# Kernel tuning notes

Hardware: AMD Instinct MI355X
Metric: run time of the kernel (lower is better)

Reference implementation:

```python
import jax, jax.numpy as jnp
import numpy as np

B, T, C = 2, 2048, 2048
N_HEAD, N_KV = 32, 8
HD = C // N_HEAD  # 64
N_REP = N_HEAD // N_KV  # 4
ROPE_BASE = 10000.0


def setup_inputs() -> dict:
    key = jax.random.key(0)
    ks = jax.random.split(key, 5)
    s = 0.02
    return {
        "x": jax.random.normal(ks[0], (B, T, C), jnp.float32),
        "Wq": jax.random.normal(ks[1], (C, N_HEAD * HD), jnp.float32) * s,
        "Wk": jax.random.normal(ks[2], (C, N_KV * HD), jnp.float32) * s,
        "Wv": jax.random.normal(ks[3], (C, N_KV * HD), jnp.float32) * s,
        "Wo": jax.random.normal(ks[4], (N_HEAD * HD, C), jnp.float32) * s,
    }


def _rope_cos_sin(seq_len, head_dim, dtype):
    inv_freq = 1.0 / (ROPE_BASE ** (jnp.arange(0, head_dim, 2, dtype=jnp.float32) / head_dim))
    t = jnp.arange(seq_len, dtype=jnp.float32)
    freqs = t[:, None] * inv_freq[None, :]           # (T, hd/2)
    emb = jnp.concatenate([freqs, freqs], axis=-1)    # (T, hd)
    return jnp.cos(emb).astype(dtype), jnp.sin(emb).astype(dtype)


def _rotate_half(x):
    h = x.shape[-1] // 2
    return jnp.concatenate([-x[..., h:], x[..., :h]], axis=-1)


def reference(x, Wq, Wk, Wv, Wo):
    b, t, c = x.shape
    # projections -> (B, H, T, hd)
    q = (x @ Wq).reshape(b, t, N_HEAD, HD).transpose(0, 2, 1, 3)
    k = (x @ Wk).reshape(b, t, N_KV, HD).transpose(0, 2, 1, 3)
    v = (x @ Wv).reshape(b, t, N_KV, HD).transpose(0, 2, 1, 3)

    cos, sin = _rope_cos_sin(t, HD, x.dtype)          # (T, hd)
    q = q * cos + _rotate_half(q) * sin
    k = k * cos + _rotate_half(k) * sin

    # GQA: group query heads (B, n_kv, n_rep, T, hd) against shared KV (no repeat materialization)
    qg = q.reshape(b, N_KV, N_REP, t, HD)
    scale = 1.0 / jnp.sqrt(jnp.asarray(HD, x.dtype))
    scores = jnp.einsum('bgrqd,bgkd->bgrqk', qg, k) * scale  # (B, n_kv, n_rep, T, T)
    causal = jnp.tril(jnp.ones((t, t), bool))
    scores = jnp.where(causal, scores, jnp.asarray(-jnp.inf, scores.dtype))
    probs = jax.nn.softmax(scores, axis=-1)
    out = jnp.einsum('bgrqk,bgkd->bgrqd', probs, v)          # (B, n_kv, n_rep, T, hd)
    out = out.reshape(b, N_HEAD, t, HD).transpose(0, 2, 1, 3).reshape(b, t, N_HEAD * HD)
    return out @ Wo
```

## Files before the change

### kernel.cpp

```cpp
#include <hip/hip_runtime.h>
#include <stdint.h>

#define Bn 2
#define Tn 2048
#define Cn 2048
#define NHEAD 32
#define NKVH 8
#define HDIM 64
#define Mn (Bn*Tn)
#define NQKV 3072
#define KOFF 2048
#define VOFF 2560

typedef __attribute__((ext_vector_type(8))) short bf16x8;
typedef __attribute__((ext_vector_type(4))) float f32x4;

#define AS1 __attribute__((address_space(1)))
#define AS3 __attribute__((address_space(3)))
#define GLOAD_LDS16(g, l) __builtin_amdgcn_global_load_lds((const AS1 void*)(g), (AS3 void*)(l), 16, 0, 0)

#define SCL 0.18033688f

#define SYNC_FENCE() __builtin_amdgcn_sched_barrier(0)
#define WAIT_VM8()  do { asm volatile("s_waitcnt vmcnt(8)" ::: "memory"); SYNC_FENCE(); } while (0)
#define WAIT_VM0()  do { asm volatile("s_waitcnt vmcnt(0)" ::: "memory"); SYNC_FENCE(); } while (0)
#define BARRIER_RAW() do { __builtin_amdgcn_s_barrier(); SYNC_FENCE(); } while (0)

__device__ __forceinline__ unsigned short f2bf(float f) {
    union { float f; unsigned u; } v; v.f = f;
    return (unsigned short)((v.u + 0x7fffu + ((v.u >> 16) & 1u)) >> 16);
}
__device__ __forceinline__ float bf2f(unsigned short b) {
    union { unsigned u; float f; } v; v.u = ((unsigned)b) << 16;
    return v.f;
}

__global__ void convert_f32_bf16(const float* __restrict__ src,
                                 unsigned short* __restrict__ dst, int n4) {
    int i = blockIdx.x * blockDim.x + threadIdx.x;
    if (i >= n4) return;
    float4 f = ((const float4*)src)[i];
    ushort4 o;
    o.x = f2bf(f.x); o.y = f2bf(f.y); o.z = f2bf(f.z); o.w = f2bf(f.w);
    ((ushort4*)dst)[i] = o;
}

__global__ void transpose_convert(const float* __restrict__ src,
                                  unsigned short* __restrict__ dst, int K, int N) {
    __shared__ float tile[32][33];
    int k0 = blockIdx.x * 32, n0 = blockIdx.y * 32;
    int tx = threadIdx.x, ty = threadIdx.y;
    #pragma unroll
    for (int yy = 0; yy < 32; yy += 8)
        tile[ty + yy][tx] = src[(size_t)(k0 + ty + yy) * N + n0 + tx];
    __syncthreads();
    #pragma unroll
    for (int yy = 0; yy < 32; yy += 8)
        dst[(size_t)(n0 + ty + yy) * K + k0 + tx] = f2bf(tile[tx][ty + yy]);
}

__global__ void transpose_wqkv(const float* __restrict__ Wq, const float* __restrict__ Wk,
                               const float* __restrict__ Wv, unsigned short* __restrict__ dst) {
    __shared__ float tile[32][33];
    int k0 = blockIdx.x * 32, n0 = blockIdx.y * 32;
    const float* src; int srcN, c0;
    if (n0 < 2048)      { src = Wq; srcN = 2048; c0 = n0; }
    else if (n0 < 2560) { src = Wk; srcN = 512;  c0 = n0 - 2048; }
    else                { src = Wv; srcN = 512;  c0 = n0 - 2560; }
    int tx = threadIdx.x, ty = threadIdx.y;
    #pragma unroll
    for (int yy = 0; yy < 32; yy += 8)
        tile[ty + yy][tx] = src[(size_t)(k0 + ty + yy) * srcN + c0 + tx];
    __syncthreads();
    #pragma unroll
    for (int yy = 0; yy < 32; yy += 8)
        dst[(size_t)(n0 + ty + yy) * Cn + k0 + tx] = f2bf(tile[tx][ty + yy]);
}

__global__ void rope_tables(float* __restrict__ ct, float* __restrict__ st) {
    int i = blockIdx.x * blockDim.x + threadIdx.x;
    int t = i >> 5, d = i & 31;
    float invf = powf(10000.0f, -(float)d / 32.0f);
    float f = (float)t * invf;
    ct[i] = cosf(f);
    st[i] = sinf(f);
}

__global__ void transpose_v(const unsigned short* __restrict__ qkv,
                            unsigned short* __restrict__ vt) {
    __shared__ unsigned short tile[32][33];
    int t0 = blockIdx.x * 32;
    int b = blockIdx.y >> 3, kvh = blockIdx.y & 7;
    int d0 = blockIdx.z * 32;
    int tx = threadIdx.x, ty = threadIdx.y;
    #pragma unroll
    for (int yy = 0; yy < 32; yy += 8)
        tile[ty + yy][tx] = qkv[(size_t)(b * Tn + t0 + ty + yy) * NQKV + VOFF + kvh * 64 + d0 + tx];
    __syncthreads();
    #pragma unroll
    for (int yy = 0; yy < 32; yy += 8)
        vt[(size_t)((b * 8 + kvh) * 64 + d0 + ty + yy) * Tn + t0 + tx] = tile[tx][ty + yy];
}

template <int BM, int BN, int WMv, int WNv, bool ROPE>
__global__ __launch_bounds__(WMv * WNv * 64, 2) void gemm_pipe(
    const unsigned short* __restrict__ A, const unsigned short* __restrict__ Bt,
    unsigned short* __restrict__ outb, float* __restrict__ outf, int N, int K,
    const float* __restrict__ ct, const float* __restrict__ st) {
    constexpr int THREADS = WMv * WNv * 64;
    constexpr int MR = BM / WMv / 16;
    constexpr int NR = BN / WNv / 16;
    constexpr int LOADS = (BM * 64 * 2) / (THREADS * 16);

    __shared__ unsigned short sA[2][BM * 64];
    __shared__ unsigned short sB[2][BN * 64];

    int tid = threadIdx.x;
    int wid = tid >> 6, lane = tid & 63;
    int wm = wid / WNv, wn = wid % WNv;
    int g = lane >> 4, r16 = lane & 15;

    int nwg = gridDim.x * gridDim.y;
    int lid = blockIdx.y * gridDim.x + blockIdx.x;
    int swz = (lid & 7) * (nwg >> 3) + (lid >> 3);
    int bx = swz % gridDim.x, by = swz / gridDim.x;
    int brow = by * BM, bcol = bx * BN;

    int NT = K / 64;

    auto stage = [&](int kt, int b) {
        #pragma unroll
        for (int li = 0; li < LOADS; li++) {
            int cb = li * (THREADS * 16) + wid * 1024;
            int bo = cb + lane * 16;
            int row = bo >> 7;
            int coff = (bo & 127) ^ ((row & 7) << 4);
            GLOAD_LDS16(A + (size_t)(brow + row) * K + kt * 64 + (coff >> 1),
                        (char*)&sA[b][0] + cb);
            GLOAD_LDS16(Bt + (size_t)(bcol + row) * K + kt * 64 + (coff >> 1),
                        (char*)&sB[b][0] + cb);
        }
    };

    f32x4 acc[MR][NR];
    #pragma unroll
    for (int m = 0; m < MR; m++)
        #pragma unroll
        for (int n = 0; n < NR; n++) acc[m][n] = (f32x4){0.f, 0.f, 0.f, 0.f};

    stage(0, 0);
    stage(1, 1);

    for (int kt = 0; kt < NT; kt++) {
        if (kt + 1 < NT) { WAIT_VM8(); } else { WAIT_VM0(); }
        BARRIER_RAW();
        const char* cA = (const char*)&sA[kt & 1][0];
        const char* cB = (const char*)&sB[kt & 1][0];
        bf16x8 av[MR][2];
        #pragma unroll
        for (int m = 0; m < MR; m++)
            #pragma unroll
            for (int kc = 0; kc < 2; kc++) {
                int row = wm * (MR * 16) + m * 16 + r16;
                int byo = (row * 128 + kc * 64 + g * 16) ^ ((row & 7) << 4);
                av[m][kc] = *(const bf16x8*)(cA + byo);
            }
        #pragma unroll
        for (int n = 0; n < NR; n++) {
            bf16x8 bv[2];
            #pragma unroll
            for (int kc = 0; kc < 2; kc++) {
                int row = wn * (NR * 16) + n * 16 + r16;
                int byo = (row * 128 + kc * 64 + g * 16) ^ ((row & 7) << 4);
                bv[kc] = *(const bf16x8*)(cB + byo);
            }
            __builtin_amdgcn_s_setprio(1);
            #pragma unroll
            for (int m = 0; m < MR; m++)
                #pragma unroll
                for (int kc = 0; kc < 2; kc++)
                    acc[m][n] = __builtin_amdgcn_mfma_f32_16x16x32_bf16(av[m][kc], bv[kc], acc[m][n], 0, 0, 0);
            __builtin_amdgcn_s_setprio(0);
        }
        BARRIER_RAW();
        if (kt + 2 < NT) stage(kt + 2, kt & 1);
        SYNC_FENCE();
    }

    if (ROPE) {
        #pragma unroll
        for (int m = 0; m < MR; m++) {
            #pragma unroll
            for (int n = 0; n < NR / 2; n++) {
                int col = bcol + wn * (NR * 16) + n * 16 + r16;
                int p = col & 63;
                bool isV = (col >= VOFF);
                float scl = (col < KOFF) ? SCL : 1.0f;
                #pragma unroll
                for (int r = 0; r < 4; r++) {
                    int row = brow + wm * (MR * 16) + m * 16 + g * 4 + r;
                    int tt = row & (Tn - 1);
                    float v0 = acc[m][n][r], v1 = acc[m][n + NR / 2][r];
                    float o0, o1;
                    if (isV) { o0 = v0; o1 = v1; }
                    else {
                        float c = ct[tt * 32 + p], s = st[tt * 32 + p];
                        o0 = (v0 * c - v1 * s) * scl;
                        o1 = (v1 * c + v0 * s) * scl;
                    }
                    outb[(size_t)row * N + col]      = f2bf(o0);
                    outb[(size_t)row * N + col + 32] = f2bf(o1);
                }
            }
        }
    } else {
        #pragma unroll
        for (int m = 0; m < MR; m++) {
            #pragma unroll
            for (int n = 0; n < NR; n++) {
                int row0 = brow + wm * (MR * 16) + m * 16 + g * 4;
                int col = bcol + wn * (NR * 16) + n * 16 + r16;
                #pragma unroll
                for (int r = 0; r < 4; r++)
                    outf[(size_t)(row0 + r) * N + col] = acc[m][n][r];
            }
        }
    }
}

__device__ __forceinline__ void flash_step(
    const bf16x8 (&qf)[2], float (&pl)[4], f32x4 (&oo)[4],
    const unsigned short* __restrict__ sK, const unsigned short* __restrict__ sVt,
    unsigned short* __restrict__ sPw, int g, int r16, int wid, bool masked) {
    f32x4 s[4];
    __builtin_amdgcn_s_setprio(1);
    #pragma unroll
    for (int n = 0; n < 4; n++) {
        s[n] = (f32x4){0.f, 0.f, 0.f, 0.f};
        #pragma unroll
        for (int kc = 0; kc < 2; kc++) {
            int kv = n * 16 + r16;
            int bo = (kv * 128 + kc * 64 + g * 16) ^ ((kv & 7) << 4);
            bf16x8 kf = *(const bf16x8*)((const char*)sK + bo);
            s[n] = __builtin_amdgcn_mfma_f32_16x16x32_bf16(qf[kc], kf, s[n], 0, 0, 0);
        }
    }
    __builtin_amdgcn_s_setprio(0);
    if (masked) {
        #pragma unroll
        for (int n = 0; n < 4; n++)
            #pragma unroll
            for (int r = 0; r < 4; r++)
                s[n][r] = (n * 16 + r16 <= wid * 16 + g * 4 + r) ? s[n][r] : -1e30f;
    }
    #pragma unroll
    for (int n = 0; n < 4; n++)
        #pragma unroll
        for (int r = 0; r < 4; r++) s[n][r] = exp2f(s[n][r]);
    #pragma unroll
    for (int r = 0; r < 4; r++)
        pl[r] += (s[0][r] + s[1][r]) + (s[2][r] + s[3][r]);
    #pragma unroll
    for (int n = 0; n < 4; n++)
        #pragma unroll
        for (int r = 0; r < 4; r++) {
            int prow = g * 4 + r;
            int bo = (prow * 128 + (n * 16 + r16) * 2) ^ ((prow & 7) << 4);
            union { float f; unsigned u; } pv; pv.f = s[n][r];
            *(unsigned short*)((char*)sPw + bo) = (unsigned short)(pv.u >> 16);
        }
    __builtin_amdgcn_s_setprio(1);
    #pragma unroll
    for (int dt = 0; dt < 4; dt++) {
        #pragma unroll
        for (int kc = 0; kc < 2; kc++) {
            int bo = (r16 * 128 + kc * 64 + g * 16) ^ ((r16 & 7) << 4);
            bf16x8 pf = *(const bf16x8*)((const char*)sPw + bo);
            int dd = dt * 16 + r16;
            int bo2 = (dd * 128 + kc * 64 + g * 16) ^ ((dd & 7) << 4);
            bf16x8 vf = *(const bf16x8*)((const char*)sVt + bo2);
            oo[dt] = __builtin_amdgcn_mfma_f32_16x16x32_bf16(pf, vf, oo[dt], 0, 0, 0);
        }
    }
    __builtin_amdgcn_s_setprio(0);
}

__global__ __launch_bounds__(256, 4) void attn_fwd(
    const unsigned short* __restrict__ qkv, const unsigned short* __restrict__ vt,
    unsigned short* __restrict__ att) {
    __shared__ unsigned short sK[2][64 * 64];
    __shared__ unsigned short sVt[2][64 * 64];
    __shared__ unsigned short sP[4][16 * 64];

    int tid = threadIdx.x;
    int wid = tid >> 6, lane = tid & 63;
    int g = lane >> 4, r16 = lane & 15;
    int qp = blockIdx.x;
    int bh = blockIdx.y;
    int b = bh >> 5, qh = bh & 31, kvh = qh >> 2;
    int qtA = qp, qtB = 31 - qp;

    const unsigned short* base = qkv + (size_t)b * Tn * NQKV;
    const unsigned short* kg = base + KOFF + kvh * 64;
    const unsigned short* vg = vt + (size_t)((b * 8 + kvh) * 64) * Tn;

    bf16x8 qfA[2], qfB[2];
    {
        int qrA = qtA * 64 + wid * 16 + r16;
        int qrB = qtB * 64 + wid * 16 + r16;
        #pragma unroll
        for (int kc = 0; kc < 2; kc++) {
            qfA[kc] = *(const bf16x8*)(base + (size_t)qrA * NQKV + qh * 64 + kc * 32 + g * 8);
            qfB[kc] = *(const bf16x8*)(base + (size_t)qrB * NQKV + qh * 64 + kc * 32 + g * 8);
        }
    }

    float plA[4], plB[4];
    f32x4 oA[4], oB[4];
    #pragma unroll
    for (int r = 0; r < 4; r++) { plA[r] = 0.f; plB[r] = 0.f; }
    #pragma unroll
    for (int d = 0; d < 4; d++) {
        oA[d] = (f32x4){0.f, 0.f, 0.f, 0.f};
        oB[d] = (f32x4){0.f, 0.f, 0.f, 0.f};
    }

    unsigned short* sPw = &sP[wid][0];

    #pragma unroll
    for (int jj = 0; jj < 2; jj++) {
        int c = wid * 2 + jj;
        int bo = c * 1024 + lane * 16;
        int row = bo >> 7;
        int coff = (bo & 127) ^ ((row & 7) << 4);
        GLOAD_LDS16(kg + (size_t)row * NQKV + (coff >> 1), (char*)&sK[0][0] + c * 1024);
        GLOAD_LDS16(vg + (size_t)row * Tn + (coff >> 1), (char*)&sVt[0][0] + c * 1024);
    }
    __syncthreads();

    int cur = 0;
    for (int j = 0; j <= qtB; j++) {
        if (j < qtB) {
            int nxt = cur ^ 1;
            #pragma unroll
            for (int jj = 0; jj < 2; jj++) {
                int c = wid * 2 + jj;
                int bo = c * 1024 + lane * 16;
                int row = bo >> 7;
                int coff = (bo & 127) ^ ((row & 7) << 4);
                GLOAD_LDS16(kg + (size_t)((j + 1) * 64 + row) * NQKV + (coff >> 1),
                            (char*)&sK[nxt][0] + c * 1024);
                GLOAD_LDS16(vg + (size_t)row * Tn + (j + 1) * 64 + (coff >> 1),
                            (char*)&sVt[nxt][0] + c * 1024);
            }
        }
        const unsigned short* sKc = &sK[cur][0];
        const unsigned short* sVc = &sVt[cur][0];
        if (j <= qtA) flash_step(qfA, plA, oA, sKc, sVc, sPw, g, r16, wid, j == qtA);
        flash_step(qfB, plB, oB, sKc, sVc, sPw, g, r16, wid, j == qtB);
        __syncthreads();
        cur ^= 1;
    }

    float lA[4], lB[4];
    #pragma unroll
    for (int r = 0; r < 4; r++) {
        float vA = plA[r], vB = plB[r];
        #pragma unroll
        for (int msk = 1; msk < 16; msk <<= 1) {
            vA += __shfl_xor(vA, msk, 64);
            vB += __shfl_xor(vB, msk, 64);
        }
        lA[r] = 1.0f / vA;
        lB[r] = 1.0f / vB;
    }
    #pragma unroll
    for (int dt = 0; dt < 4; dt++)
        #pragma unroll
        for (int r = 0; r < 4; r++) {
            int qgA = qtA * 64 + wid * 16 + g * 4 + r;
            int qgB = qtB * 64 + wid * 16 + g * 4 + r;
            att[(size_t)(b * Tn + qgA) * Cn + qh * 64 + dt * 16 + r16] = f2bf(oA[dt][r] * lA[r]);
            att[(size_t)(b * Tn + qgB) * Cn + qh * 64 + dt * 16 + r16] = f2bf(oB[dt][r] * lB[r]);
        }
}

extern "C" void kernel_launch(void* const* d_in, const int* in_sizes, int n_in,
                              void* d_out, int out_size, void* d_ws, size_t ws_size,
                              hipStream_t stream) {
    const float* x  = (const float*)d_in[0];
    const float* Wq = (const float*)d_in[1];
    const float* Wk = (const float*)d_in[2];
    const float* Wv = (const float*)d_in[3];
    const float* Wo = (const float*)d_in[4];
    float* out = (float*)d_out;

    char* w = (char*)d_ws;
    unsigned short* Xb    = (unsigned short*)w; w += (size_t)Mn * Cn * 2;
    unsigned short* Wqkvt = (unsigned short*)w; w += (size_t)NQKV * Cn * 2;
    unsigned short* Wot   = (unsigned short*)w; w += (size_t)Cn * Cn * 2;
    unsigned short* QKV   = (unsigned short*)w; w += (size_t)Mn * NQKV * 2;
    unsigned short* ATT   = (unsigned short*)w; w += (size_t)Mn * Cn * 2;
    unsigned short* Vt    = (unsigned short*)w; w += (size_t)Bn * NKVH * HDIM * Tn * 2;
    float* ct = (float*)w; w += (size_t)Tn * 32 * 4;
    float* st = (float*)w; w += (size_t)Tn * 32 * 4;

    convert_f32_bf16<<<(Mn * Cn / 4) / 256, 256, 0, stream>>>(x, Xb, Mn * Cn / 4);
    dim3 tb(32, 8);
    transpose_wqkv<<<dim3(64, 96), tb, 0, stream>>>(Wq, Wk, Wv, Wqkvt);
    transpose_convert<<<dim3(64, 64), tb, 0, stream>>>(Wo, Wot, Cn, 2048);
    rope_tables<<<(Tn * 32) / 256, 256, 0, stream>>>(ct, st);

    gemm_pipe<256, 256, 2, 4, true><<<dim3(NQKV / 256, Mn / 256), 512, 0, stream>>>(
        Xb, Wqkvt, QKV, nullptr, NQKV, Cn, ct, st);
    transpose_v<<<dim3(Tn / 32, Bn * NKVH, 2), tb, 0, stream>>>(QKV, Vt);
    attn_fwd<<<dim3(16, Bn * NHEAD), 256, 0, stream>>>(QKV, Vt, ATT);
    gemm_pipe<128, 128, 2, 2, false><<<dim3(Cn / 128, Mn / 128), 256, 0, stream>>>(
        ATT, Wot, nullptr, out, Cn, Cn, nullptr, nullptr);
}
```

Measured before the change: 223.8 us.

## Rewrite QKV GEMM with phased quarter-tile MFMA schedule interleaving global loads

Replaces the templated 256x256 QKV projection GEMM with a dedicated kernel. It splits each K-tile into four quadrant MFMA phases and issues half-tile global-to-LDS loads for the next stage between phases, with barriers and LDS waits around each phase. The aim is finer overlap of memory traffic with MFMA work and fewer register-held fragments at once. The cost is many more barriers per tile, plus a full vmcnt(0) wait at each tile boundary that could serialize loads. The output projection GEMM is split into its own non-template copy with no functional change.

```diff
diff --git a/kernel.cpp b/kernel.cpp
--- a/kernel.cpp
+++ b/kernel.cpp
@@ -22,8 +22,9 @@
 #define SCL 0.18033688f
 
 #define SYNC_FENCE() __builtin_amdgcn_sched_barrier(0)
-#define WAIT_VM8()  do { asm volatile("s_waitcnt vmcnt(8)" ::: "memory"); SYNC_FENCE(); } while (0)
-#define WAIT_VM0()  do { asm volatile("s_waitcnt vmcnt(0)" ::: "memory"); SYNC_FENCE(); } while (0)
+#define WAIT_VM8()   do { asm volatile("s_waitcnt vmcnt(8)" ::: "memory"); SYNC_FENCE(); } while (0)
+#define WAIT_VM0()   do { asm volatile("s_waitcnt vmcnt(0)" ::: "memory"); SYNC_FENCE(); } while (0)
+#define WAIT_LGKM0() do { asm volatile("s_waitcnt lgkmcnt(0)" ::: "memory"); SYNC_FENCE(); } while (0)
 #define BARRIER_RAW() do { __builtin_amdgcn_s_barrier(); SYNC_FENCE(); } while (0)
 
 __device__ __forceinline__ unsigned short f2bf(float f) {
@@ -102,36 +103,171 @@
         vt[(size_t)((b * 8 + kvh) * 64 + d0 + ty + yy) * Tn + t0 + tx] = tile[tx][ty + yy];
 }
 
-template <int BM, int BN, int WMv, int WNv, bool ROPE>
-__global__ __launch_bounds__(WMv * WNv * 64, 2) void gemm_pipe(
+#define MFMA_Q(MH, NH, AV, BV) do { \
+    __builtin_amdgcn_s_setprio(1); \
+    _Pragma("unroll") for (int n_ = 0; n_ < 2; n_++) \
+    _Pragma("unroll") for (int m_ = 0; m_ < 4; m_++) \
+    _Pragma("unroll") for (int kc_ = 0; kc_ < 2; kc_++) \
+        acc[(MH) * 4 + m_][(NH) * 2 + n_] = __builtin_amdgcn_mfma_f32_16x16x32_bf16( \
+            AV[m_][kc_], BV[n_][kc_], acc[(MH) * 4 + m_][(NH) * 2 + n_], 0, 0, 0); \
+    __builtin_amdgcn_s_setprio(0); \
+} while (0)
+
+#define TILE4(SLOT, ST_EN, ST_KT) do { \
+    const char* cSA = (const char*)&sA[SLOT][0]; \
+    const char* cSB = (const char*)&sB[SLOT][0]; \
+     \
+    load_av(av0, cSA, 0); load_bv(bv, cSB, 0); \
+    if (ST_EN) stage_half(A, sA, (SLOT) ^ 1, brow, ST_KT, 0); \
+    BARRIER_RAW(); WAIT_LGKM0(); \
+    MFMA_Q(0, 0, av0, bv); \
+    BARRIER_RAW(); \
+     \
+    load_av(av1, cSA, 1); \
+    if (ST_EN) stage_half(A, sA, (SLOT) ^ 1, brow, ST_KT, 1); \
+    BARRIER_RAW(); WAIT_LGKM0(); \
+    MFMA_Q(1, 0, av1, bv); \
+    BARRIER_RAW(); \
+     \
+    load_bv(bv, cSB, 1); \
+    if (ST_EN) stage_half(Bt, sB, (SLOT) ^ 1, bcol, ST_KT, 0); \
+    BARRIER_RAW(); WAIT_LGKM0(); \
+    MFMA_Q(0, 1, av0, bv); \
+    BARRIER_RAW(); \
+     \
+    if (ST_EN) stage_half(Bt, sB, (SLOT) ^ 1, bcol, ST_KT, 1); \
+    BARRIER_RAW(); \
+    MFMA_Q(1, 1, av1, bv); \
+} while (0)
+
+__global__ __launch_bounds__(512, 2) void gemm256_8ph(
     const unsigned short* __restrict__ A, const unsigned short* __restrict__ Bt,
-    unsigned short* __restrict__ outb, float* __restrict__ outf, int N, int K,
+    unsigned short* __restrict__ outb,
     const float* __restrict__ ct, const float* __restrict__ st) {
-    constexpr int THREADS = WMv * WNv * 64;
-    constexpr int MR = BM / WMv / 16;
-    constexpr int NR = BN / WNv / 16;
-    constexpr int LOADS = (BM * 64 * 2) / (THREADS * 16);
-
-    __shared__ unsigned short sA[2][BM * 64];
-    __shared__ unsigned short sB[2][BN * 64];
-
+    __shared__ unsigned short sA[2][256 * 64];
+    __shared__ unsigned short sB[2][256 * 64];
     int tid = threadIdx.x;
     int wid = tid >> 6, lane = tid & 63;
-    int wm = wid / WNv, wn = wid % WNv;
+    int wm = wid >> 2, wn = wid & 3;
     int g = lane >> 4, r16 = lane & 15;
 
     int nwg = gridDim.x * gridDim.y;
     int lid = blockIdx.y * gridDim.x + blockIdx.x;
     int swz = (lid & 7) * (nwg >> 3) + (lid >> 3);
     int bx = swz % gridDim.x, by = swz / gridDim.x;
-    int brow = by * BM, bcol = bx * BN;
+    int brow = by * 256, bcol = bx * 256;
+
+    const int NT = Cn / 64;
+
+    auto stage_half = [&](const unsigned short* __restrict__ src, unsigned short (*dst)[256 * 64],
+                          int sl, int base_row, int kt, int h) {
+        #pragma unroll
+        for (int r = 0; r < 2; r++) {
+            int off = h * 16384 + r * 8192 + wid * 1024 + lane * 16;
+            int row = off >> 7;
+            int coff = (off & 127) ^ ((row & 7) << 4);
+            GLOAD_LDS16(src + (size_t)(base_row + row) * Cn + kt * 64 + (coff >> 1),
+                        (char*)&dst[sl][0] + h * 16384 + r * 8192 + wid * 1024);
+        }
+    };
+    auto load_av = [&](bf16x8 (&av)[4][2], const char* cS, int mh) {
+        #pragma unroll
+        for (int m = 0; m < 4; m++)
+            #pragma unroll
+            for (int kc = 0; kc < 2; kc++) {
+                int row = wm * 128 + mh * 64 + m * 16 + r16;
+                int byo = (row * 128 + kc * 64 + g * 16) ^ ((row & 7) << 4);
+                av[m][kc] = *(const bf16x8*)(cS + byo);
+            }
+    };
+    auto load_bv = [&](bf16x8 (&bv)[2][2], const char* cS, int nh) {
+        #pragma unroll
+        for (int n = 0; n < 2; n++)
+            #pragma unroll
+            for (int kc = 0; kc < 2; kc++) {
+                int row = wn * 64 + nh * 32 + n * 16 + r16;
+                int byo = (row * 128 + kc * 64 + g * 16) ^ ((row & 7) << 4);
+                bv[n][kc] = *(const bf16x8*)(cS + byo);
+            }
+    };
+
+    f32x4 acc[8][4];
+    #pragma unroll
+    for (int m = 0; m < 8; m++)
+        #pragma unroll
+        for (int n = 0; n < 4; n++) acc[m][n] = (f32x4){0.f, 0.f, 0.f, 0.f};
+    bf16x8 av0[4][2], av1[4][2], bv[2][2];
+
+    #pragma unroll
+    for (int h = 0; h < 2; h++) {
+        stage_half(A, sA, 0, brow, 0, h);
+        stage_half(Bt, sB, 0, bcol, 0, h);
+    }
+    WAIT_VM0();
+    BARRIER_RAW();
+
+    for (int i = 0; i < NT / 2; i++) {
+        int t0 = 2 * i;
+        TILE4(0, true, t0 + 1);
+        WAIT_VM0();
+        BARRIER_RAW();
+        bool en = (t0 + 2 < NT);
+        TILE4(1, en, t0 + 2);
+        WAIT_VM0();
+        BARRIER_RAW();
+    }
+
+    #pragma unroll
+    for (int m = 0; m < 8; m++) {
+        #pragma unroll
+        for (int n = 0; n < 2; n++) {
+            int col = bcol + wn * 64 + n * 16 + r16;
+            int p = col & 63;
+            bool isV = (col >= VOFF);
+            float scl = (col < KOFF) ? SCL : 1.0f;
+            #pragma unroll
+            for (int r = 0; r < 4; r++) {
+                int row = brow + wm * 128 + m * 16 + g * 4 + r;
+                int tt = row & (Tn - 1);
+                float v0 = acc[m][n][r], v1 = acc[m][n + 2][r];
+                float o0, o1;
+                if (isV) { o0 = v0; o1 = v1; }
+                else {
+                    float c = ct[tt * 32 + p], s = st[tt * 32 + p];
+                    o0 = (v0 * c - v1 * s) * scl;
+                    o1 = (v1 * c + v0 * s) * scl;
+                }
+                outb[(size_t)row * NQKV + col]      = f2bf(o0);
+                outb[(size_t)row * NQKV + col + 32] = f2bf(o1);
+            }
+        }
+    }
+}
+
+__global__ __launch_bounds__(256, 2) void gemm_pipe128(
+    const unsigned short* __restrict__ A, const unsigned short* __restrict__ Bt,
+    float* __restrict__ outf, int N, int K) {
+    constexpr int MR = 4, NR = 4, LOADS = 4;
+    __shared__ unsigned short sA[2][128 * 64];
+    __shared__ unsigned short sB[2][128 * 64];
+
+    int tid = threadIdx.x;
+    int wid = tid >> 6, lane = tid & 63;
+    int wm = wid >> 1, wn = wid & 1;
+    int g = lane >> 4, r16 = lane & 15;
+
+    int nwg = gridDim.x * gridDim.y;
+    int lid = blockIdx.y * gridDim.x + blockIdx.x;
+    int swz = (lid & 7) * (nwg >> 3) + (lid >> 3);
+    int bx = swz % gridDim.x, by = swz / gridDim.x;
+    int brow = by * 128, bcol = bx * 128;
 
     int NT = K / 64;
 
     auto stage = [&](int kt, int b) {
         #pragma unroll
         for (int li = 0; li < LOADS; li++) {
-            int cb = li * (THREADS * 16) + wid * 1024;
+            int cb = li * 4096 + wid * 1024;
             int bo = cb + lane * 16;
             int row = bo >> 7;
             int coff = (bo & 127) ^ ((row & 7) << 4);
@@ -161,25 +297,25 @@
         for (int m = 0; m < MR; m++)
             #pragma unroll
             for (int kc = 0; kc < 2; kc++) {
-                int row = wm * (MR * 16) + m * 16 + r16;
+                int row = wm * 64 + m * 16 + r16;
                 int byo = (row * 128 + kc * 64 + g * 16) ^ ((row & 7) << 4);
                 av[m][kc] = *(const bf16x8*)(cA + byo);
             }
         #pragma unroll
         for (int n = 0; n < NR; n++) {
-            bf16x8 bv[2];
+            bf16x8 bvv[2];
             #pragma unroll
             for (int kc = 0; kc < 2; kc++) {
-                int row = wn * (NR * 16) + n * 16 + r16;
+                int row = wn * 64 + n * 16 + r16;
                 int byo = (row * 128 + kc * 64 + g * 16) ^ ((row & 7) << 4);
-                bv[kc] = *(const bf16x8*)(cB + byo);
+                bvv[kc] = *(const bf16x8*)(cB + byo);
             }
             __builtin_amdgcn_s_setprio(1);
             #pragma unroll
             for (int m = 0; m < MR; m++)
                 #pragma unroll
                 for (int kc = 0; kc < 2; kc++)
-                    acc[m][n] = __builtin_amdgcn_mfma_f32_16x16x32_bf16(av[m][kc], bv[kc], acc[m][n], 0, 0, 0);
+                    acc[m][n] = __builtin_amdgcn_mfma_f32_16x16x32_bf16(av[m][kc], bvv[kc], acc[m][n], 0, 0, 0);
             __builtin_amdgcn_s_setprio(0);
         }
         BARRIER_RAW();
@@ -187,45 +323,16 @@
         SYNC_FENCE();
     }
 
-    if (ROPE) {
-        #pragma unroll
-        for (int m = 0; m < MR; m++) {
-            #pragma unroll
-            for (int n = 0; n < NR / 2; n++) {
-                int col = bcol + wn * (NR * 16) + n * 16 + r16;
-                int p = col & 63;
-                bool isV = (col >= VOFF);
-                float scl = (col < KOFF) ? SCL : 1.0f;
-                #pragma unroll
-                for (int r = 0; r < 4; r++) {
-                    int row = brow + wm * (MR * 16) + m * 16 + g * 4 + r;
-                    int tt = row & (Tn - 1);
-                    float v0 = acc[m][n][r], v1 = acc[m][n + NR / 2][r];
-                    float o0, o1;
-                    if (isV) { o0 = v0; o1 = v1; }
-                    else {
-                        float c = ct[tt * 32 + p], s = st[tt * 32 + p];
-                        o0 = (v0 * c - v1 * s) * scl;
-                        o1 = (v1 * c + v0 * s) * scl;
-                    }
-                    outb[(size_t)row * N + col]      = f2bf(o0);
-                    outb[(size_t)row * N + col + 32] = f2bf(o1);
-                }
-            }
-        }
-    } else {
-        #pragma unroll
-        for (int m = 0; m < MR; m++) {
-            #pragma unroll
-            for (int n = 0; n < NR; n++) {
-                int row0 = brow + wm * (MR * 16) + m * 16 + g * 4;
-                int col = bcol + wn * (NR * 16) + n * 16 + r16;
-                #pragma unroll
-                for (int r = 0; r < 4; r++)
-                    outf[(size_t)(row0 + r) * N + col] = acc[m][n][r];
-            }
-        }
-    }
+    #pragma unroll
+    for (int m = 0; m < MR; m++)
+        #pragma unroll
+        for (int n = 0; n < NR; n++) {
+            int row0 = brow + wm * 64 + m * 16 + g * 4;
+            int col = bcol + wn * 64 + n * 16 + r16;
+            #pragma unroll
+            for (int r = 0; r < 4; r++)
+                outf[(size_t)(row0 + r) * N + col] = acc[m][n][r];
+        }
 }
 
 __device__ __forceinline__ void flash_step(
@@ -411,10 +518,8 @@
     transpose_convert<<<dim3(64, 64), tb, 0, stream>>>(Wo, Wot, Cn, 2048);
     rope_tables<<<(Tn * 32) / 256, 256, 0, stream>>>(ct, st);
 
-    gemm_pipe<256, 256, 2, 4, true><<<dim3(NQKV / 256, Mn / 256), 512, 0, stream>>>(
-        Xb, Wqkvt, QKV, nullptr, NQKV, Cn, ct, st);
+    gemm256_8ph<<<dim3(NQKV / 256, Mn / 256), 512, 0, stream>>>(Xb, Wqkvt, QKV, ct, st);
     transpose_v<<<dim3(Tn / 32, Bn * NKVH, 2), tb, 0, stream>>>(QKV, Vt);
     attn_fwd<<<dim3(16, Bn * NHEAD), 256, 0, stream>>>(QKV, Vt, ATT);
-    gemm_pipe<128, 128, 2, 2, false><<<dim3(Cn / 128, Mn / 128), 256, 0, stream>>>(
-        ATT, Wot, nullptr, out, Cn, Cn, nullptr, nullptr);
-}
+    gemm_pipe128<<<dim3(Cn / 128, Mn / 128), 256, 0, stream>>>(ATT, Wot, out, Cn, Cn);
+}
```

New measurement: 241.6 us. 1.08x slower.

## Read K and V tiles directly from global memory in attention, dropping LDS staging

Applied to the files above, without the earlier changes.

The attention kernel no longer stages K and V^T tiles into double-buffered shared memory with async global-to-LDS loads and per-tile barriers. Each wave now loads its MFMA fragments for K and V straight from global memory (through cache) on every step, and the s_setprio hints are removed. This removes the block-wide barriers and the LDS footprint but makes every wave re-fetch the same K/V data and exposes global-load latency to the MFMA chain without explicit prefetch.

```diff
diff --git a/kernel.cpp b/kernel.cpp
--- a/kernel.cpp
+++ b/kernel.cpp
@@ -230,22 +230,18 @@
 
 __device__ __forceinline__ void flash_step(
     const bf16x8 (&qf)[2], float (&pl)[4], f32x4 (&oo)[4],
-    const unsigned short* __restrict__ sK, const unsigned short* __restrict__ sVt,
-    unsigned short* __restrict__ sPw, int g, int r16, int wid, bool masked) {
+    const unsigned short* __restrict__ kg, const unsigned short* __restrict__ vg,
+    unsigned short* __restrict__ sPw, int j, int g, int r16, int wid, bool masked) {
     f32x4 s[4];
-    __builtin_amdgcn_s_setprio(1);
     #pragma unroll
     for (int n = 0; n < 4; n++) {
         s[n] = (f32x4){0.f, 0.f, 0.f, 0.f};
         #pragma unroll
         for (int kc = 0; kc < 2; kc++) {
-            int kv = n * 16 + r16;
-            int bo = (kv * 128 + kc * 64 + g * 16) ^ ((kv & 7) << 4);
-            bf16x8 kf = *(const bf16x8*)((const char*)sK + bo);
+            const bf16x8 kf = *(const bf16x8*)(kg + (size_t)(j * 64 + n * 16 + r16) * NQKV + kc * 32 + g * 8);
             s[n] = __builtin_amdgcn_mfma_f32_16x16x32_bf16(qf[kc], kf, s[n], 0, 0, 0);
         }
     }
-    __builtin_amdgcn_s_setprio(0);
     if (masked) {
         #pragma unroll
         for (int n = 0; n < 4; n++)
@@ -269,27 +265,21 @@
             union { float f; unsigned u; } pv; pv.f = s[n][r];
             *(unsigned short*)((char*)sPw + bo) = (unsigned short)(pv.u >> 16);
         }
-    __builtin_amdgcn_s_setprio(1);
     #pragma unroll
     for (int dt = 0; dt < 4; dt++) {
         #pragma unroll
         for (int kc = 0; kc < 2; kc++) {
             int bo = (r16 * 128 + kc * 64 + g * 16) ^ ((r16 & 7) << 4);
             bf16x8 pf = *(const bf16x8*)((const char*)sPw + bo);
-            int dd = dt * 16 + r16;
-            int bo2 = (dd * 128 + kc * 64 + g * 16) ^ ((dd & 7) << 4);
-            bf16x8 vf = *(const bf16x8*)((const char*)sVt + bo2);
+            const bf16x8 vf = *(const bf16x8*)(vg + (size_t)(dt * 16 + r16) * Tn + j * 64 + kc * 32 + g * 8);
             oo[dt] = __builtin_amdgcn_mfma_f32_16x16x32_bf16(pf, vf, oo[dt], 0, 0, 0);
         }
     }
-    __builtin_amdgcn_s_setprio(0);
 }
 
 __global__ __launch_bounds__(256, 4) void attn_fwd(
     const unsigned short* __restrict__ qkv, const unsigned short* __restrict__ vt,
     unsigned short* __restrict__ att) {
-    __shared__ unsigned short sK[2][64 * 64];
-    __shared__ unsigned short sVt[2][64 * 64];
     __shared__ unsigned short sP[4][16 * 64];
 
     int tid = threadIdx.x;
@@ -327,39 +317,9 @@
 
     unsigned short* sPw = &sP[wid][0];
 
-    #pragma unroll
-    for (int jj = 0; jj < 2; jj++) {
-        int c = wid * 2 + jj;
-        int bo = c * 1024 + lane * 16;
-        int row = bo >> 7;
-        int coff = (bo & 127) ^ ((row & 7) << 4);
-        GLOAD_LDS16(kg + (size_t)row * NQKV + (coff >> 1), (char*)&sK[0][0] + c * 1024);
-        GLOAD_LDS16(vg + (size_t)row * Tn + (coff >> 1), (char*)&sVt[0][0] + c * 1024);
-    }
-    __syncthreads();
-
-    int cur = 0;
     for (int j = 0; j <= qtB; j++) {
-        if (j < qtB) {
-            int nxt = cur ^ 1;
-            #pragma unroll
-            for (int jj = 0; jj < 2; jj++) {
-                int c = wid * 2 + jj;
-                int bo = c * 1024 + lane * 16;
-                int row = bo >> 7;
-                int coff = (bo & 127) ^ ((row & 7) << 4);
-                GLOAD_LDS16(kg + (size_t)((j + 1) * 64 + row) * NQKV + (coff >> 1),
-                            (char*)&sK[nxt][0] + c * 1024);
-                GLOAD_LDS16(vg + (size_t)row * Tn + (j + 1) * 64 + (coff >> 1),
-                            (char*)&sVt[nxt][0] + c * 1024);
-            }
-        }
-        const unsigned short* sKc = &sK[cur][0];
-        const unsigned short* sVc = &sVt[cur][0];
-        if (j <= qtA) flash_step(qfA, plA, oA, sKc, sVc, sPw, g, r16, wid, j == qtA);
-        flash_step(qfB, plB, oB, sKc, sVc, sPw, g, r16, wid, j == qtB);
-        __syncthreads();
-        cur ^= 1;
+        if (j <= qtA) flash_step(qfA, plA, oA, kg, vg, sPw, j, g, r16, wid, j == qtA);
+        flash_step(qfB, plB, oB, kg, vg, sPw, j, g, r16, wid, j == qtB);
     }
 
     float lA[4], lB[4];
```

New measurement: 387.4 us. +73.1%, slower.

## Fuse both causal query tiles per KV step and drop K/V double buffering

Applied to the files above, without the earlier changes.

Adds a fused flash step that computes the QK^T, softmax-exp and PV MFMAs for both paired query tiles (A and B) against one shared K/V tile, interleaving their instructions for more ILP. Each wave gets separate P scratch buffers so the two tiles' probabilities don't collide. K/V staging changes from a prefetching double buffer to a single buffer that is loaded and synchronised before each step. This cuts LDS use, but global-to-LDS loads are no longer overlapped with compute, and the loop now has two barriers per iteration.

```diff
diff --git a/kernel.cpp b/kernel.cpp
--- a/kernel.cpp
+++ b/kernel.cpp
@@ -228,7 +228,74 @@
     }
 }
 
-__device__ __forceinline__ void flash_step(
+__device__ __forceinline__ void flash_fused(
+    const bf16x8 (&qfA)[2], const bf16x8 (&qfB)[2],
+    float (&plA)[4], float (&plB)[4], f32x4 (&oA)[4], f32x4 (&oB)[4],
+    const unsigned short* __restrict__ sK, const unsigned short* __restrict__ sVt,
+    unsigned short* __restrict__ sP0, unsigned short* __restrict__ sP1,
+    int g, int r16, int wid, bool maskedA) {
+    f32x4 sa[4], sb[4];
+    __builtin_amdgcn_s_setprio(1);
+    #pragma unroll
+    for (int n = 0; n < 4; n++) {
+        sa[n] = (f32x4){0.f, 0.f, 0.f, 0.f};
+        sb[n] = (f32x4){0.f, 0.f, 0.f, 0.f};
+        #pragma unroll
+        for (int kc = 0; kc < 2; kc++) {
+            int kv = n * 16 + r16;
+            int bo = (kv * 128 + kc * 64 + g * 16) ^ ((kv & 7) << 4);
+            bf16x8 kf = *(const bf16x8*)((const char*)sK + bo);
+            sa[n] = __builtin_amdgcn_mfma_f32_16x16x32_bf16(qfA[kc], kf, sa[n], 0, 0, 0);
+            sb[n] = __builtin_amdgcn_mfma_f32_16x16x32_bf16(qfB[kc], kf, sb[n], 0, 0, 0);
+        }
+    }
+    __builtin_amdgcn_s_setprio(0);
+    if (maskedA) {
+        #pragma unroll
+        for (int n = 0; n < 4; n++)
+            #pragma unroll
+            for (int r = 0; r < 4; r++)
+                sa[n][r] = (n * 16 + r16 <= wid * 16 + g * 4 + r) ? sa[n][r] : -1e30f;
+    }
+    #pragma unroll
+    for (int n = 0; n < 4; n++)
+        #pragma unroll
+        for (int r = 0; r < 4; r++) { sa[n][r] = exp2f(sa[n][r]); sb[n][r] = exp2f(sb[n][r]); }
+    #pragma unroll
+    for (int r = 0; r < 4; r++) {
+        plA[r] += (sa[0][r] + sa[1][r]) + (sa[2][r] + sa[3][r]);
+        plB[r] += (sb[0][r] + sb[1][r]) + (sb[2][r] + sb[3][r]);
+    }
+    #pragma unroll
+    for (int n = 0; n < 4; n++)
+        #pragma unroll
+        for (int r = 0; r < 4; r++) {
+            int prow = g * 4 + r;
+            int bo = (prow * 128 + (n * 16 + r16) * 2) ^ ((prow & 7) << 4);
+            union { float f; unsigned u; } pa; pa.f = sa[n][r];
+            union { float f; unsigned u; } pb; pb.f = sb[n][r];
+            *(unsigned short*)((char*)sP0 + bo) = (unsigned short)(pa.u >> 16);
+            *(unsigned short*)((char*)sP1 + bo) = (unsigned short)(pb.u >> 16);
+        }
+    __builtin_amdgcn_s_setprio(1);
+    #pragma unroll
+    for (int dt = 0; dt < 4; dt++) {
+        #pragma unroll
+        for (int kc = 0; kc < 2; kc++) {
+            int bo = (r16 * 128 + kc * 64 + g * 16) ^ ((r16 & 7) << 4);
+            bf16x8 pfA = *(const bf16x8*)((const char*)sP0 + bo);
+            bf16x8 pfB = *(const bf16x8*)((const char*)sP1 + bo);
+            int dd = dt * 16 + r16;
+            int bo2 = (dd * 128 + kc * 64 + g * 16) ^ ((dd & 7) << 4);
+            bf16x8 vf = *(const bf16x8*)((const char*)sVt + bo2);
+            oA[dt] = __builtin_amdgcn_mfma_f32_16x16x32_bf16(pfA, vf, oA[dt], 0, 0, 0);
+            oB[dt] = __builtin_amdgcn_mfma_f32_16x16x32_bf16(pfB, vf, oB[dt], 0, 0, 0);
+        }
+    }
+    __builtin_amdgcn_s_setprio(0);
+}
+
+__device__ __forceinline__ void flash_single(
     const bf16x8 (&qf)[2], float (&pl)[4], f32x4 (&oo)[4],
     const unsigned short* __restrict__ sK, const unsigned short* __restrict__ sVt,
     unsigned short* __restrict__ sPw, int g, int r16, int wid, bool masked) {
@@ -288,9 +355,9 @@
 __global__ __launch_bounds__(256, 4) void attn_fwd(
     const unsigned short* __restrict__ qkv, const unsigned short* __restrict__ vt,
     unsigned short* __restrict__ att) {
-    __shared__ unsigned short sK[2][64 * 64];
-    __shared__ unsigned short sVt[2][64 * 64];
-    __shared__ unsigned short sP[4][16 * 64];
+    __shared__ unsigned short sK[64 * 64];
+    __shared__ unsigned short sVt[64 * 64];
+    __shared__ unsigned short sP[4][2][16 * 64];
 
     int tid = threadIdx.x;
     int wid = tid >> 6, lane = tid & 63;
@@ -325,41 +392,26 @@
         oB[d] = (f32x4){0.f, 0.f, 0.f, 0.f};
     }
 
-    unsigned short* sPw = &sP[wid][0];
-
-    #pragma unroll
-    for (int jj = 0; jj < 2; jj++) {
-        int c = wid * 2 + jj;
-        int bo = c * 1024 + lane * 16;
-        int row = bo >> 7;
-        int coff = (bo & 127) ^ ((row & 7) << 4);
-        GLOAD_LDS16(kg + (size_t)row * NQKV + (coff >> 1), (char*)&sK[0][0] + c * 1024);
-        GLOAD_LDS16(vg + (size_t)row * Tn + (coff >> 1), (char*)&sVt[0][0] + c * 1024);
-    }
-    __syncthreads();
-
-    int cur = 0;
+    unsigned short* sP0 = &sP[wid][0][0];
+    unsigned short* sP1 = &sP[wid][1][0];
+
     for (int j = 0; j <= qtB; j++) {
-        if (j < qtB) {
-            int nxt = cur ^ 1;
-            #pragma unroll
-            for (int jj = 0; jj < 2; jj++) {
-                int c = wid * 2 + jj;
-                int bo = c * 1024 + lane * 16;
-                int row = bo >> 7;
-                int coff = (bo & 127) ^ ((row & 7) << 4);
-                GLOAD_LDS16(kg + (size_t)((j + 1) * 64 + row) * NQKV + (coff >> 1),
-                            (char*)&sK[nxt][0] + c * 1024);
-                GLOAD_LDS16(vg + (size_t)row * Tn + (j + 1) * 64 + (coff >> 1),
-                            (char*)&sVt[nxt][0] + c * 1024);
-            }
-        }
-        const unsigned short* sKc = &sK[cur][0];
-        const unsigned short* sVc = &sVt[cur][0];
-        if (j <= qtA) flash_step(qfA, plA, oA, sKc, sVc, sPw, g, r16, wid, j == qtA);
-        flash_step(qfB, plB, oB, sKc, sVc, sPw, g, r16, wid, j == qtB);
         __syncthreads();
-        cur ^= 1;
+        #pragma unroll
+        for (int jj = 0; jj < 2; jj++) {
+            int c = wid * 2 + jj;
+            int bo = c * 1024 + lane * 16;
+            int row = bo >> 7;
+            int coff = (bo & 127) ^ ((row & 7) << 4);
+            GLOAD_LDS16(kg + (size_t)(j * 64 + row) * NQKV + (coff >> 1), (char*)sK + c * 1024);
+            GLOAD_LDS16(vg + (size_t)row * Tn + j * 64 + (coff >> 1), (char*)sVt + c * 1024);
+        }
+        __syncthreads();
+
+        if (j <= qtA)
+            flash_fused(qfA, qfB, plA, plB, oA, oB, sK, sVt, sP0, sP1, g, r16, wid, j == qtA);
+        else
+            flash_single(qfB, plB, oB, sK, sVt, sP1, g, r16, wid, j == qtB);
     }
 
     float lA[4], lB[4];
```

Result: slower. 254.5 us (+13.7%).
